# Optimization experiments

Measured on AMD Instinct MI355X. Metric: run time of the kernel, lower is better.

Reference implementation:

```python
import jax, jax.numpy as jnp
import numpy as np

B, T, C, H = 4, 2048, 768, 12
D = C // H

def setup_inputs() -> dict:
    key = jax.random.key(0)
    ks = jax.random.split(key, 8)
    s = 1.0 / np.sqrt(C)
    return {
        "x":  jax.random.normal(ks[0], (B, T, C), dtype=jnp.float32),
        "Wq": jax.random.normal(ks[1], (C, C), dtype=jnp.float32) * s,
        "bq": jax.random.normal(ks[2], (C,), dtype=jnp.float32) * 0.02,
        "Wk": jax.random.normal(ks[3], (C, C), dtype=jnp.float32) * s,
        "bk": jax.random.normal(ks[4], (C,), dtype=jnp.float32) * 0.02,
        "Wv": jax.random.normal(ks[5], (C, C), dtype=jnp.float32) * s,
        "bv": jax.random.normal(ks[6], (C,), dtype=jnp.float32) * 0.02,
        "Wp": jax.random.normal(ks[7], (C, C), dtype=jnp.float32) * s,
    }

def reference(x, Wq, bq, Wk, bk, Wv, bv, Wp):
    # Linear projections (torch Linear: y = x @ W.T + b)
    q = x @ Wq.T + bq
    k = x @ Wk.T + bk
    v = x @ Wv.T + bv
    # [B,T,C] -> [B,H,T,D]
    q = q.reshape(B, T, H, D).transpose(0, 2, 1, 3)
    k = k.reshape(B, T, H, D).transpose(0, 2, 1, 3)
    v = v.reshape(B, T, H, D).transpose(0, 2, 1, 3)
    scale = 1.0 / np.sqrt(D).astype(np.float32)
    scores = jnp.einsum('bhqd,bhkd->bhqk', q, k) * scale  # [B,H,T,T]
    attn = jax.nn.softmax(scores, axis=-1)  # no mask in original module
    out = jnp.einsum('bhqk,bhkd->bhqd', attn, v)
    out = out.transpose(0, 2, 1, 3).reshape(B, T, C)
    return out @ Wp.T  # proj has bias=False
```

## Files before the change

kernel.cpp:

```cpp
#include <hip/hip_runtime.h>
#include <hip/hip_bf16.h>
#include <cmath>

constexpr int B  = 4;
constexpr int T  = 2048;
constexpr int C  = 768;
constexpr int H  = 12;
constexpr int Dh = 64;
constexpr int M  = B * T;
constexpr int NQKV = 3 * C;
constexpr int WS2  = C * C;

typedef short bf16x8 __attribute__((ext_vector_type(8)));
typedef short bf16x4 __attribute__((ext_vector_type(4)));
typedef float f32x4  __attribute__((ext_vector_type(4)));
typedef float f32x16 __attribute__((ext_vector_type(16)));

constexpr float SOFT_SCALE = 0.18033688011112042f;

__device__ inline short f2bf(float f) {
    unsigned u = __float_as_uint(f);
    u += 0x7fffu + ((u >> 16) & 1u);
    return (short)(u >> 16);
}

__device__ inline unsigned pk_bf16(float a, float b) {
    __hip_bfloat162 h = __float22bfloat162_rn(float2{a, b});
    return *(unsigned*)&h;
}

__device__ inline bf16x8 mk8(unsigned a, unsigned b, unsigned c, unsigned d) {
    union { unsigned u[4]; bf16x8 v; } x;
    x.u[0] = a; x.u[1] = b; x.u[2] = c; x.u[3] = d;
    return x.v;
}

typedef const __attribute__((address_space(1))) unsigned GU;
typedef __attribute__((address_space(3))) unsigned LU;
__device__ inline void async_copy16(const void* g, void* l) {
    __builtin_amdgcn_global_load_lds((GU*)g, (LU*)l, 16, 0, 0);
}

constexpr size_t XE = (size_t)M * C;
constexpr size_t CV_TOTAL = XE + 4 * (size_t)WS2;

__global__ __launch_bounds__(256)
void convert_all(const float* __restrict__ x,  const float* __restrict__ Wq,
                 const float* __restrict__ Wk, const float* __restrict__ Wv,
                 const float* __restrict__ Wp,
                 short* __restrict__ xb, short* __restrict__ Wqkv,
                 short* __restrict__ Wpb) {
    size_t i = ((size_t)blockIdx.x * 256 + threadIdx.x) * 4;
    const float* src; short* dst; size_t off;
    if (i < XE)                        { src = x;  dst = xb;            off = i; }
    else if (i < XE + WS2)             { src = Wq; dst = Wqkv;          off = i - XE; }
    else if (i < XE + 2 * (size_t)WS2) { src = Wk; dst = Wqkv + WS2;    off = i - XE - WS2; }
    else if (i < XE + 3 * (size_t)WS2) { src = Wv; dst = Wqkv + 2 * WS2; off = i - XE - 2 * (size_t)WS2; }
    else                               { src = Wp; dst = Wpb;           off = i - XE - 3 * (size_t)WS2; }
    float4 v = *(const float4*)(src + off);
    bf16x4 o; o[0] = f2bf(v.x); o[1] = f2bf(v.y); o[2] = f2bf(v.z); o[3] = f2bf(v.w);
    *(bf16x4*)(dst + off) = o;
}

constexpr int BM = 128;
constexpr int MTILES = M / BM;

template<int BN_, int WMW, int WNW, int OUT_BF16, int QSCALE>
__global__ __launch_bounds__(256)
void gemm_bt(const short* __restrict__ A, const short* __restrict__ W,
             const float* __restrict__ bias0, const float* __restrict__ bias1,
             const float* __restrict__ bias2,
             void* __restrict__ Yv, int Ndim, int Kdim) {
    constexpr int MT  = BM / WMW / 16;
    constexpr int NT  = BN_ / WNW / 16;
    constexpr int NCH = (BM + BN_) / 16;

    __shared__ short As[2][BM * 32];
    __shared__ short Bs[2][BN_ * 32];

    const int tid  = threadIdx.x;
    const int wave = tid >> 6;
    const int lane = tid & 63;
    const int li   = lane & 15;
    const int quad = lane >> 4;
    const int wm   = wave % WMW;
    const int wn   = wave / WMW;

    const int ntiles = Ndim / BN_;
    const int bid  = blockIdx.x;
    const int xcd  = bid & 7;
    const int idx  = bid >> 3;
    const int mloc = idx / ntiles;
    const int ntt  = idx % ntiles;
    const int m0   = (xcd * (MTILES / 8) + mloc) * BM;
    const int n0   = ntt * BN_;

    f32x4 acc[MT][NT];
    #pragma unroll
    for (int i = 0; i < MT; ++i)
        #pragma unroll
        for (int j = 0; j < NT; ++j)
            acc[i][j] = (f32x4){0.f, 0.f, 0.f, 0.f};

    const int lrow = lane >> 2;
    const int lkof = (lane & 3) * 8;

    for (int k0 = 0; k0 < Kdim; k0 += 64) {
        __syncthreads();
        #pragma unroll
        for (int h = 0; h < 2; ++h)
            #pragma unroll
            for (int ii = 0; ii < NCH / 4; ++ii) {
                int c = ii * 4 + wave;
                if (c < BM / 16)
                    async_copy16(A + (size_t)(m0 + c * 16 + lrow) * Kdim
                                   + k0 + h * 32 + lkof,
                                 &As[h][c * 512]);
                else
                    async_copy16(W + (size_t)(n0 + (c - BM / 16) * 16 + lrow) * Kdim
                                   + k0 + h * 32 + lkof,
                                 &Bs[h][(c - BM / 16) * 512]);
            }
        __syncthreads();

        #pragma unroll
        for (int h = 0; h < 2; ++h) {
            bf16x8 af[MT], bfr[NT];
            #pragma unroll
            for (int t = 0; t < MT; ++t)
                af[t] = *(const bf16x8*)&As[h][(wm * MT * 16 + t * 16 + li) * 32 + quad * 8];
            #pragma unroll
            for (int t = 0; t < NT; ++t)
                bfr[t] = *(const bf16x8*)&Bs[h][(wn * NT * 16 + t * 16 + li) * 32 + quad * 8];
            #pragma unroll
            for (int i = 0; i < MT; ++i)
                #pragma unroll
                for (int j = 0; j < NT; ++j)
                    acc[i][j] = __builtin_amdgcn_mfma_f32_16x16x32_bf16(
                        af[i], bfr[j], acc[i][j], 0, 0, 0);
        }
    }

    float bb[NT];
    #pragma unroll
    for (int nt = 0; nt < NT; ++nt) bb[nt] = 0.f;
    if (bias0) {
        int s = n0 / C;
        const float* bp = (s == 0) ? bias0 : ((s == 1) ? bias1 : bias2);
        int nb = n0 % C;
        #pragma unroll
        for (int nt = 0; nt < NT; ++nt)
            bb[nt] = bp[nb + wn * NT * 16 + nt * 16 + li];
    }

    #pragma unroll
    for (int mt = 0; mt < MT; ++mt)
        #pragma unroll
        for (int nt = 0; nt < NT; ++nt)
            #pragma unroll
            for (int r = 0; r < 4; ++r) {
                int row = m0 + wm * MT * 16 + mt * 16 + quad * 4 + r;
                int col = n0 + wn * NT * 16 + nt * 16 + li;
                float v = acc[mt][nt][r] + bb[nt];
                if constexpr (QSCALE) {
                    if (n0 < C) v *= SOFT_SCALE;
                }
                if constexpr (OUT_BF16)
                    ((short*)Yv)[(size_t)row * Ndim + col] = f2bf(v);
                else
                    ((float*)Yv)[(size_t)row * Ndim + col] = v;
            }
}

constexpr int QT   = 128;
constexpr int KTT  = 64;
constexpr int LSTR = 72;
constexpr int QS   = NQKV;

__global__ __launch_bounds__(256, 3)
void attn_fwd(const short* __restrict__ QKV, short* __restrict__ O) {
    __shared__ short Ks0[KTT * LSTR];
    __shared__ short Ks1[KTT * LSTR];
    __shared__ short Vt0[Dh * LSTR];
    __shared__ short Vt1[Dh * LSTR];

    const int tid  = threadIdx.x;
    const int wave = tid >> 6;
    const int lane = tid & 63;
    const int r31  = lane & 31;
    const int hi   = lane >> 5;

    const int bid   = blockIdx.x;
    const int xcd   = bid & 7;
    const int idx   = bid >> 3;
    const int gloc  = idx >> 4;
    const int qt    = idx & 15;
    const int group = xcd * 6 + gloc;
    const int b     = group / H;
    const int h     = group % H;
    const int qw    = qt * QT + wave * 32;

    const short* Qg = QKV + (size_t)(b * T) * QS + h * Dh;
    const short* Kg = QKV + (size_t)(b * T) * QS + C + h * Dh;
    const short* Vg = QKV + (size_t)(b * T) * QS + 2 * C + h * Dh;

    bf16x8 qf[4];
    #pragma unroll
    for (int f = 0; f < 4; ++f)
        qf[f] = *(const bf16x8*)(Qg + (size_t)(qw + r31) * QS + f * 16 + hi * 8);

    bf16x8 ones;
    #pragma unroll
    for (int i = 0; i < 8; ++i) ones[i] = (short)0x3F80;

    f32x16 oacc0 = (f32x16)(0.f);
    f32x16 oacc1 = (f32x16)(0.f);
    f32x16 lacc  = (f32x16)(0.f);

    const int ktok = tid >> 3;
    const int kch  = tid & 7;
    const int vd2  = (tid & 31) * 2;
    const int vg   = tid >> 5;

    int4 kpre[2];
    unsigned vpre[8];

    auto load_regs = [&](int kt0) {
        kpre[0] = *(const int4*)(Kg + (size_t)(kt0 + ktok)      * QS + kch * 8);
        kpre[1] = *(const int4*)(Kg + (size_t)(kt0 + ktok + 32) * QS + kch * 8);
        #pragma unroll
        for (int t2 = 0; t2 < 8; ++t2)
            vpre[t2] = *(const unsigned*)(Vg + (size_t)(kt0 + vg * 8 + t2) * QS + vd2);
    };
    auto write_tile = [&](short (&KsT)[KTT * LSTR], short (&VtT)[Dh * LSTR]) {
        *(int4*)&KsT[ktok * LSTR + kch * 8]        = kpre[0];
        *(int4*)&KsT[(ktok + 32) * LSTR + kch * 8] = kpre[1];
        unsigned lo[4], hh[4];
        #pragma unroll
        for (int j = 0; j < 4; ++j) {
            lo[j] = __builtin_amdgcn_perm(vpre[2 * j + 1], vpre[2 * j], 0x05040100u);
            hh[j] = __builtin_amdgcn_perm(vpre[2 * j + 1], vpre[2 * j], 0x07060302u);
        }
        *(int4*)&VtT[vd2 * LSTR + vg * 8]       = make_int4(lo[0], lo[1], lo[2], lo[3]);
        *(int4*)&VtT[(vd2 + 1) * LSTR + vg * 8] = make_int4(hh[0], hh[1], hh[2], hh[3]);
    };

    auto half_iter = [&](const short (&KsT)[KTT * LSTR], const short (&VtT)[Dh * LSTR],
                         short (&KsN)[KTT * LSTR], short (&VtN)[Dh * LSTR],
                         bool do_stage, int next_load) {
        __syncthreads();

        f32x16 st0 = (f32x16)(0.f);
        f32x16 st1 = (f32x16)(0.f);
        __builtin_amdgcn_s_setprio(1);
        #pragma unroll
        for (int f = 0; f < 4; ++f) {
            bf16x8 k0 = *(const bf16x8*)&KsT[(r31)      * LSTR + f * 16 + hi * 8];
            bf16x8 k1 = *(const bf16x8*)&KsT[(32 + r31) * LSTR + f * 16 + hi * 8];
            st0 = __builtin_amdgcn_mfma_f32_32x32x16_bf16(k0, qf[f], st0, 0, 0, 0);
            st1 = __builtin_amdgcn_mfma_f32_32x32x16_bf16(k1, qf[f], st1, 0, 0, 0);
        }
        __builtin_amdgcn_s_setprio(0);

        if (do_stage)       write_tile(KsN, VtN);
        if (next_load >= 0) load_regs(next_load);

        #pragma unroll
        for (int kb = 0; kb < 2; ++kb) {
            f32x16 s = kb ? st1 : st0;
            unsigned d[8];
            #pragma unroll
            for (int j = 0; j < 8; ++j) {
                float pa = __builtin_amdgcn_exp2f(s[2 * j]);
                float pb = __builtin_amdgcn_exp2f(s[2 * j + 1]);
                d[j] = pk_bf16(pa, pb);
            }
            auto s02 = __builtin_amdgcn_permlane32_swap(d[0], d[2], false, false);
            auto s13 = __builtin_amdgcn_permlane32_swap(d[1], d[3], false, false);
            auto s46 = __builtin_amdgcn_permlane32_swap(d[4], d[6], false, false);
            auto s57 = __builtin_amdgcn_permlane32_swap(d[5], d[7], false, false);
            bf16x8 pf0 = mk8(s02[0], s13[0], s02[1], s13[1]);
            bf16x8 pf1 = mk8(s46[0], s57[0], s46[1], s57[1]);

            __builtin_amdgcn_s_setprio(1);
            lacc = __builtin_amdgcn_mfma_f32_32x32x16_bf16(pf0, ones, lacc, 0, 0, 0);
            lacc = __builtin_amdgcn_mfma_f32_32x32x16_bf16(pf1, ones, lacc, 0, 0, 0);

            bf16x8 v00 = *(const bf16x8*)&VtT[(r31)      * LSTR + kb * 32 + hi * 8];
            bf16x8 v01 = *(const bf16x8*)&VtT[(r31)      * LSTR + kb * 32 + 16 + hi * 8];
            bf16x8 v10 = *(const bf16x8*)&VtT[(32 + r31) * LSTR + kb * 32 + hi * 8];
            bf16x8 v11 = *(const bf16x8*)&VtT[(32 + r31) * LSTR + kb * 32 + 16 + hi * 8];
            oacc0 = __builtin_amdgcn_mfma_f32_32x32x16_bf16(pf0, v00, oacc0, 0, 0, 0);
            oacc0 = __builtin_amdgcn_mfma_f32_32x32x16_bf16(pf1, v01, oacc0, 0, 0, 0);
            oacc1 = __builtin_amdgcn_mfma_f32_32x32x16_bf16(pf0, v10, oacc1, 0, 0, 0);
            oacc1 = __builtin_amdgcn_mfma_f32_32x32x16_bf16(pf1, v11, oacc1, 0, 0, 0);
            __builtin_amdgcn_s_setprio(0);
        }
    };

    load_regs(0);
    write_tile(Ks0, Vt0);
    load_regs(KTT);

    for (int kt = 0; kt < T; kt += 2 * KTT) {
        half_iter(Ks0, Vt0, Ks1, Vt1, true,
                  (kt + 2 * KTT < T) ? kt + 2 * KTT : -1);
        half_iter(Ks1, Vt1, Ks0, Vt0, kt + 2 * KTT < T,
                  (kt + 3 * KTT < T) ? kt + 3 * KTT : -1);
    }

    #pragma unroll
    for (int r = 0; r < 16; ++r) {
        float inv = 1.0f / lacc[r];
        int row = (r & 3) + 8 * (r >> 2) + 4 * hi;
        short* op = O + (size_t)(b * T + qw + row) * C + h * Dh + r31;
        op[0]  = f2bf(oacc0[r] * inv);
        op[32] = f2bf(oacc1[r] * inv);
    }
}

extern "C" void kernel_launch(void* const* d_in, const int* in_sizes, int n_in,
                              void* d_out, int out_size, void* d_ws, size_t ws_size,
                              hipStream_t stream) {
    (void)in_sizes; (void)n_in; (void)out_size; (void)ws_size;

    const float* x  = (const float*)d_in[0];
    const float* Wq = (const float*)d_in[1];
    const float* bq = (const float*)d_in[2];
    const float* Wk = (const float*)d_in[3];
    const float* bk = (const float*)d_in[4];
    const float* Wv = (const float*)d_in[5];
    const float* bv = (const float*)d_in[6];
    const float* Wp = (const float*)d_in[7];
    float* out = (float*)d_out;

    short* xb    = (short*)d_ws;
    short* Wqkv  = xb + (size_t)M * C;
    short* Wpb   = Wqkv + 3 * (size_t)WS2;
    short* QKVb  = Wpb + (size_t)WS2;
    short* AOb   = QKVb + (size_t)M * NQKV;

    convert_all<<<dim3(CV_TOTAL / 1024), 256, 0, stream>>>(
        x, Wq, Wk, Wv, Wp, xb, Wqkv, Wpb);

    gemm_bt<128, 2, 2, 1, 1><<<dim3(MTILES * (NQKV / 128)), 256, 0, stream>>>(
        xb, Wqkv, bq, bk, bv, QKVb, NQKV, C);

    attn_fwd<<<dim3((T / QT) * H * B), 256, 0, stream>>>(QKVb, AOb);

    gemm_bt<64, 4, 1, 0, 0><<<dim3(MTILES * (C / 64)), 256, 0, stream>>>(
        AOb, Wpb, nullptr, nullptr, nullptr, out, C, C);
}
```

Before: 232.3 us.

## Add 256x256-tile QKV GEMM kernel with 512 threads and XCD-aware block mapping

Replaces the generic 128-tile QKV projection GEMM with a dedicated kernel that uses 256x256 output tiles, 8 waves, double-buffered async LDS staging over 64-wide K chunks, and a block-to-tile mapping that groups M-rows per XCD. Larger tiles raise arithmetic intensity and cut redundant global loads of A and W, and the XCD grouping aims to improve L2 locality. The trade-offs are heavy LDS use (128 KB per block) and high register pressure from 32 accumulators per wave, which limit occupancy, plus only 288 blocks to spread across the CUs.

```diff
diff --git a/kernel.cpp b/kernel.cpp
--- a/kernel.cpp
+++ b/kernel.cpp
@@ -172,6 +172,110 @@
             }
 }
 
+__global__ __launch_bounds__(512, 2)
+void gemm_qkv256(const short* __restrict__ A, const short* __restrict__ W,
+                 const float* __restrict__ bias0, const float* __restrict__ bias1,
+                 const float* __restrict__ bias2,
+                 short* __restrict__ Y) {
+    constexpr int Kdim = C;
+    constexpr int Ndim = NQKV;
+    constexpr int MT = 8, NT = 4;
+
+    __shared__ short As0[2][256 * 32];
+    __shared__ short As1[2][256 * 32];
+    __shared__ short Bs0[2][256 * 32];
+    __shared__ short Bs1[2][256 * 32];
+
+    const int tid  = threadIdx.x;
+    const int wave = tid >> 6;
+    const int lane = tid & 63;
+    const int li   = lane & 15;
+    const int quad = lane >> 4;
+    const int wm   = wave >> 2;
+    const int wn   = wave & 3;
+
+    const int bid  = blockIdx.x;
+    const int xcd  = bid & 7;
+    const int idx  = bid >> 3;
+    const int m0   = (xcd * 4 + idx / 9) * 256;
+    const int n0   = (idx % 9) * 256;
+
+    f32x4 acc[MT][NT];
+    #pragma unroll
+    for (int i = 0; i < MT; ++i)
+        #pragma unroll
+        for (int j = 0; j < NT; ++j)
+            acc[i][j] = (f32x4){0.f, 0.f, 0.f, 0.f};
+
+    const int grow = tid >> 2;
+    const int gcol = (tid & 3) * 8;
+    auto stage = [&](short (&Ad)[2][256 * 32], short (&Bd)[2][256 * 32], int k0) {
+        #pragma unroll
+        for (int h = 0; h < 2; ++h)
+            #pragma unroll
+            for (int r = 0; r < 2; ++r) {
+                async_copy16(A + (size_t)(m0 + r * 128 + grow) * Kdim
+                               + k0 + h * 32 + gcol,
+                             &Ad[h][(r * 128 + wave * 16) * 32]);
+                async_copy16(W + (size_t)(n0 + r * 128 + grow) * Kdim
+                               + k0 + h * 32 + gcol,
+                             &Bd[h][(r * 128 + wave * 16) * 32]);
+            }
+    };
+
+    auto compute = [&](const short (&Ad)[2][256 * 32],
+                       const short (&Bd)[2][256 * 32]) {
+        #pragma unroll
+        for (int h = 0; h < 2; ++h) {
+            bf16x8 af[MT], bfr[NT];
+            #pragma unroll
+            for (int t = 0; t < MT; ++t)
+                af[t] = *(const bf16x8*)&Ad[h][(wm * 128 + t * 16 + li) * 32 + quad * 8];
+            #pragma unroll
+            for (int t = 0; t < NT; ++t)
+                bfr[t] = *(const bf16x8*)&Bd[h][(wn * 64 + t * 16 + li) * 32 + quad * 8];
+            #pragma unroll
+            for (int i = 0; i < MT; ++i)
+                #pragma unroll
+                for (int j = 0; j < NT; ++j)
+                    acc[i][j] = __builtin_amdgcn_mfma_f32_16x16x32_bf16(
+                        af[i], bfr[j], acc[i][j], 0, 0, 0);
+        }
+    };
+
+    stage(As0, Bs0, 0);
+    for (int i = 0; i < 6; ++i) {
+        const int k0 = i * 128;
+        __syncthreads();
+        stage(As1, Bs1, k0 + 64);
+        compute(As0, Bs0);
+        __syncthreads();
+        if (i < 5) stage(As0, Bs0, k0 + 128);
+        compute(As1, Bs1);
+    }
+
+    const int s  = n0 / C;
+    const float* bp = (s == 0) ? bias0 : ((s == 1) ? bias1 : bias2);
+    const int nb = n0 % C;
+    float bb[NT];
+    #pragma unroll
+    for (int nt = 0; nt < NT; ++nt)
+        bb[nt] = bp[nb + wn * 64 + nt * 16 + li];
+
+    #pragma unroll
+    for (int mt = 0; mt < MT; ++mt)
+        #pragma unroll
+        for (int nt = 0; nt < NT; ++nt)
+            #pragma unroll
+            for (int r = 0; r < 4; ++r) {
+                int row = m0 + wm * 128 + mt * 16 + quad * 4 + r;
+                int col = n0 + wn * 64 + nt * 16 + li;
+                float v = acc[mt][nt][r] + bb[nt];
+                if (n0 < C) v *= SOFT_SCALE;
+                Y[(size_t)row * Ndim + col] = f2bf(v);
+            }
+}
+
 constexpr int QT   = 128;
 constexpr int KTT  = 64;
 constexpr int LSTR = 72;
@@ -343,8 +447,8 @@
     convert_all<<<dim3(CV_TOTAL / 1024), 256, 0, stream>>>(
         x, Wq, Wk, Wv, Wp, xb, Wqkv, Wpb);
 
-    gemm_bt<128, 2, 2, 1, 1><<<dim3(MTILES * (NQKV / 128)), 256, 0, stream>>>(
-        xb, Wqkv, bq, bk, bv, QKVb, NQKV, C);
+    gemm_qkv256<<<dim3(288), 512, 0, stream>>>(
+        xb, Wqkv, bq, bk, bv, QKVb);
 
     attn_fwd<<<dim3((T / QT) * H * B), 256, 0, stream>>>(QKVb, AOb);
 
```

After: 240.8 us. 1.04x slower.

## Give each attention wave two 32-row query groups, halving block size

Applied to the files above, without the earlier changes.

The attention kernel now runs 2 waves per block instead of 4, and each wave handles 64 query rows as two 32-row groups. Each K and V fragment read from LDS is reused across both groups, which cuts LDS reads per unit of MFMA work. The K/V staging loads per thread double to keep the same 64-token tile. The cost is higher register pressure, since accumulators and Q fragments double, and fewer waves per block to hide latency.

```diff
diff --git a/kernel.cpp b/kernel.cpp
--- a/kernel.cpp
+++ b/kernel.cpp
@@ -177,7 +177,7 @@
 constexpr int LSTR = 72;
 constexpr int QS   = NQKV;
 
-__global__ __launch_bounds__(256, 3)
+__global__ __launch_bounds__(128, 2)
 void attn_fwd(const short* __restrict__ QKV, short* __restrict__ O) {
     __shared__ short Ks0[KTT * LSTR];
     __shared__ short Ks1[KTT * LSTR];
@@ -198,51 +198,62 @@
     const int group = xcd * 6 + gloc;
     const int b     = group / H;
     const int h     = group % H;
-    const int qw    = qt * QT + wave * 32;
+    const int qw    = qt * QT + wave * 64;
 
     const short* Qg = QKV + (size_t)(b * T) * QS + h * Dh;
     const short* Kg = QKV + (size_t)(b * T) * QS + C + h * Dh;
     const short* Vg = QKV + (size_t)(b * T) * QS + 2 * C + h * Dh;
 
-    bf16x8 qf[4];
-    #pragma unroll
-    for (int f = 0; f < 4; ++f)
-        qf[f] = *(const bf16x8*)(Qg + (size_t)(qw + r31) * QS + f * 16 + hi * 8);
+    bf16x8 qf[2][4];
+    #pragma unroll
+    for (int qg = 0; qg < 2; ++qg)
+        #pragma unroll
+        for (int f = 0; f < 4; ++f)
+            qf[qg][f] = *(const bf16x8*)(Qg + (size_t)(qw + qg * 32 + r31) * QS
+                                            + f * 16 + hi * 8);
 
     bf16x8 ones;
     #pragma unroll
     for (int i = 0; i < 8; ++i) ones[i] = (short)0x3F80;
 
-    f32x16 oacc0 = (f32x16)(0.f);
-    f32x16 oacc1 = (f32x16)(0.f);
-    f32x16 lacc  = (f32x16)(0.f);
+    f32x16 oacc0[2], oacc1[2], lacc[2];
+    #pragma unroll
+    for (int qg = 0; qg < 2; ++qg) {
+        oacc0[qg] = (f32x16)(0.f);
+        oacc1[qg] = (f32x16)(0.f);
+        lacc[qg]  = (f32x16)(0.f);
+    }
 
     const int ktok = tid >> 3;
     const int kch  = tid & 7;
     const int vd2  = (tid & 31) * 2;
     const int vg   = tid >> 5;
 
-    int4 kpre[2];
-    unsigned vpre[8];
+    int4 kpre[4];
+    unsigned vpre[16];
 
     auto load_regs = [&](int kt0) {
-        kpre[0] = *(const int4*)(Kg + (size_t)(kt0 + ktok)      * QS + kch * 8);
-        kpre[1] = *(const int4*)(Kg + (size_t)(kt0 + ktok + 32) * QS + kch * 8);
-        #pragma unroll
-        for (int t2 = 0; t2 < 8; ++t2)
-            vpre[t2] = *(const unsigned*)(Vg + (size_t)(kt0 + vg * 8 + t2) * QS + vd2);
+        #pragma unroll
+        for (int r = 0; r < 4; ++r)
+            kpre[r] = *(const int4*)(Kg + (size_t)(kt0 + ktok + r * 16) * QS + kch * 8);
+        #pragma unroll
+        for (int t2 = 0; t2 < 16; ++t2)
+            vpre[t2] = *(const unsigned*)(Vg + (size_t)(kt0 + vg * 16 + t2) * QS + vd2);
     };
     auto write_tile = [&](short (&KsT)[KTT * LSTR], short (&VtT)[Dh * LSTR]) {
-        *(int4*)&KsT[ktok * LSTR + kch * 8]        = kpre[0];
-        *(int4*)&KsT[(ktok + 32) * LSTR + kch * 8] = kpre[1];
-        unsigned lo[4], hh[4];
-        #pragma unroll
-        for (int j = 0; j < 4; ++j) {
+        #pragma unroll
+        for (int r = 0; r < 4; ++r)
+            *(int4*)&KsT[(ktok + r * 16) * LSTR + kch * 8] = kpre[r];
+        unsigned lo[8], hh[8];
+        #pragma unroll
+        for (int j = 0; j < 8; ++j) {
             lo[j] = __builtin_amdgcn_perm(vpre[2 * j + 1], vpre[2 * j], 0x05040100u);
             hh[j] = __builtin_amdgcn_perm(vpre[2 * j + 1], vpre[2 * j], 0x07060302u);
         }
-        *(int4*)&VtT[vd2 * LSTR + vg * 8]       = make_int4(lo[0], lo[1], lo[2], lo[3]);
-        *(int4*)&VtT[(vd2 + 1) * LSTR + vg * 8] = make_int4(hh[0], hh[1], hh[2], hh[3]);
+        *(int4*)&VtT[vd2 * LSTR + vg * 16]           = make_int4(lo[0], lo[1], lo[2], lo[3]);
+        *(int4*)&VtT[vd2 * LSTR + vg * 16 + 8]       = make_int4(lo[4], lo[5], lo[6], lo[7]);
+        *(int4*)&VtT[(vd2 + 1) * LSTR + vg * 16]     = make_int4(hh[0], hh[1], hh[2], hh[3]);
+        *(int4*)&VtT[(vd2 + 1) * LSTR + vg * 16 + 8] = make_int4(hh[4], hh[5], hh[6], hh[7]);
     };
 
     auto half_iter = [&](const short (&KsT)[KTT * LSTR], const short (&VtT)[Dh * LSTR],
@@ -250,51 +261,56 @@
                          bool do_stage, int next_load) {
         __syncthreads();
 
-        f32x16 st0 = (f32x16)(0.f);
-        f32x16 st1 = (f32x16)(0.f);
-        __builtin_amdgcn_s_setprio(1);
-        #pragma unroll
-        for (int f = 0; f < 4; ++f) {
-            bf16x8 k0 = *(const bf16x8*)&KsT[(r31)      * LSTR + f * 16 + hi * 8];
-            bf16x8 k1 = *(const bf16x8*)&KsT[(32 + r31) * LSTR + f * 16 + hi * 8];
-            st0 = __builtin_amdgcn_mfma_f32_32x32x16_bf16(k0, qf[f], st0, 0, 0, 0);
-            st1 = __builtin_amdgcn_mfma_f32_32x32x16_bf16(k1, qf[f], st1, 0, 0, 0);
-        }
-        __builtin_amdgcn_s_setprio(0);
-
-        if (do_stage)       write_tile(KsN, VtN);
-        if (next_load >= 0) load_regs(next_load);
-
-        #pragma unroll
-        for (int kb = 0; kb < 2; ++kb) {
-            f32x16 s = kb ? st1 : st0;
-            unsigned d[8];
-            #pragma unroll
-            for (int j = 0; j < 8; ++j) {
-                float pa = __builtin_amdgcn_exp2f(s[2 * j]);
-                float pb = __builtin_amdgcn_exp2f(s[2 * j + 1]);
-                d[j] = pk_bf16(pa, pb);
-            }
-            auto s02 = __builtin_amdgcn_permlane32_swap(d[0], d[2], false, false);
-            auto s13 = __builtin_amdgcn_permlane32_swap(d[1], d[3], false, false);
-            auto s46 = __builtin_amdgcn_permlane32_swap(d[4], d[6], false, false);
-            auto s57 = __builtin_amdgcn_permlane32_swap(d[5], d[7], false, false);
-            bf16x8 pf0 = mk8(s02[0], s13[0], s02[1], s13[1]);
-            bf16x8 pf1 = mk8(s46[0], s57[0], s46[1], s57[1]);
-
+        #pragma unroll
+        for (int qg = 0; qg < 2; ++qg) {
+            f32x16 st0 = (f32x16)(0.f);
+            f32x16 st1 = (f32x16)(0.f);
             __builtin_amdgcn_s_setprio(1);
-            lacc = __builtin_amdgcn_mfma_f32_32x32x16_bf16(pf0, ones, lacc, 0, 0, 0);
-            lacc = __builtin_amdgcn_mfma_f32_32x32x16_bf16(pf1, ones, lacc, 0, 0, 0);
-
-            bf16x8 v00 = *(const bf16x8*)&VtT[(r31)      * LSTR + kb * 32 + hi * 8];
-            bf16x8 v01 = *(const bf16x8*)&VtT[(r31)      * LSTR + kb * 32 + 16 + hi * 8];
-            bf16x8 v10 = *(const bf16x8*)&VtT[(32 + r31) * LSTR + kb * 32 + hi * 8];
-            bf16x8 v11 = *(const bf16x8*)&VtT[(32 + r31) * LSTR + kb * 32 + 16 + hi * 8];
-            oacc0 = __builtin_amdgcn_mfma_f32_32x32x16_bf16(pf0, v00, oacc0, 0, 0, 0);
-            oacc0 = __builtin_amdgcn_mfma_f32_32x32x16_bf16(pf1, v01, oacc0, 0, 0, 0);
-            oacc1 = __builtin_amdgcn_mfma_f32_32x32x16_bf16(pf0, v10, oacc1, 0, 0, 0);
-            oacc1 = __builtin_amdgcn_mfma_f32_32x32x16_bf16(pf1, v11, oacc1, 0, 0, 0);
+            #pragma unroll
+            for (int f = 0; f < 4; ++f) {
+                bf16x8 k0 = *(const bf16x8*)&KsT[(r31)      * LSTR + f * 16 + hi * 8];
+                bf16x8 k1 = *(const bf16x8*)&KsT[(32 + r31) * LSTR + f * 16 + hi * 8];
+                st0 = __builtin_amdgcn_mfma_f32_32x32x16_bf16(k0, qf[qg][f], st0, 0, 0, 0);
+                st1 = __builtin_amdgcn_mfma_f32_32x32x16_bf16(k1, qf[qg][f], st1, 0, 0, 0);
+            }
             __builtin_amdgcn_s_setprio(0);
+
+            if (qg == 0) {
+                if (do_stage)       write_tile(KsN, VtN);
+                if (next_load >= 0) load_regs(next_load);
+            }
+
+            #pragma unroll
+            for (int kb = 0; kb < 2; ++kb) {
+                f32x16 s = kb ? st1 : st0;
+                unsigned d[8];
+                #pragma unroll
+                for (int j = 0; j < 8; ++j) {
+                    float pa = __builtin_amdgcn_exp2f(s[2 * j]);
+                    float pb = __builtin_amdgcn_exp2f(s[2 * j + 1]);
+                    d[j] = pk_bf16(pa, pb);
+                }
+                auto s02 = __builtin_amdgcn_permlane32_swap(d[0], d[2], false, false);
+                auto s13 = __builtin_amdgcn_permlane32_swap(d[1], d[3], false, false);
+                auto s46 = __builtin_amdgcn_permlane32_swap(d[4], d[6], false, false);
+                auto s57 = __builtin_amdgcn_permlane32_swap(d[5], d[7], false, false);
+                bf16x8 pf0 = mk8(s02[0], s13[0], s02[1], s13[1]);
+                bf16x8 pf1 = mk8(s46[0], s57[0], s46[1], s57[1]);
+
+                __builtin_amdgcn_s_setprio(1);
+                lacc[qg] = __builtin_amdgcn_mfma_f32_32x32x16_bf16(pf0, ones, lacc[qg], 0, 0, 0);
+                lacc[qg] = __builtin_amdgcn_mfma_f32_32x32x16_bf16(pf1, ones, lacc[qg], 0, 0, 0);
+
+                bf16x8 v00 = *(const bf16x8*)&VtT[(r31)      * LSTR + kb * 32 + hi * 8];
+                bf16x8 v01 = *(const bf16x8*)&VtT[(r31)      * LSTR + kb * 32 + 16 + hi * 8];
+                bf16x8 v10 = *(const bf16x8*)&VtT[(32 + r31) * LSTR + kb * 32 + hi * 8];
+                bf16x8 v11 = *(const bf16x8*)&VtT[(32 + r31) * LSTR + kb * 32 + 16 + hi * 8];
+                oacc0[qg] = __builtin_amdgcn_mfma_f32_32x32x16_bf16(pf0, v00, oacc0[qg], 0, 0, 0);
+                oacc0[qg] = __builtin_amdgcn_mfma_f32_32x32x16_bf16(pf1, v01, oacc0[qg], 0, 0, 0);
+                oacc1[qg] = __builtin_amdgcn_mfma_f32_32x32x16_bf16(pf0, v10, oacc1[qg], 0, 0, 0);
+                oacc1[qg] = __builtin_amdgcn_mfma_f32_32x32x16_bf16(pf1, v11, oacc1[qg], 0, 0, 0);
+                __builtin_amdgcn_s_setprio(0);
+            }
         }
     };
 
@@ -310,13 +326,15 @@
     }
 
     #pragma unroll
-    for (int r = 0; r < 16; ++r) {
-        float inv = 1.0f / lacc[r];
-        int row = (r & 3) + 8 * (r >> 2) + 4 * hi;
-        short* op = O + (size_t)(b * T + qw + row) * C + h * Dh + r31;
-        op[0]  = f2bf(oacc0[r] * inv);
-        op[32] = f2bf(oacc1[r] * inv);
-    }
+    for (int qg = 0; qg < 2; ++qg)
+        #pragma unroll
+        for (int r = 0; r < 16; ++r) {
+            float inv = 1.0f / lacc[qg][r];
+            int row = (r & 3) + 8 * (r >> 2) + 4 * hi;
+            short* op = O + (size_t)(b * T + qw + qg * 32 + row) * C + h * Dh + r31;
+            op[0]  = f2bf(oacc0[qg][r] * inv);
+            op[32] = f2bf(oacc1[qg][r] * inv);
+        }
 }
 
 extern "C" void kernel_launch(void* const* d_in, const int* in_sizes, int n_in,
@@ -346,7 +364,7 @@
     gemm_bt<128, 2, 2, 1, 1><<<dim3(MTILES * (NQKV / 128)), 256, 0, stream>>>(
         xb, Wqkv, bq, bk, bv, QKVb, NQKV, C);
 
-    attn_fwd<<<dim3((T / QT) * H * B), 256, 0, stream>>>(QKVb, AOb);
+    attn_fwd<<<dim3((T / QT) * H * B), 128, 0, stream>>>(QKVb, AOb);
 
     gemm_bt<64, 4, 1, 0, 0><<<dim3(MTILES * (C / 64)), 256, 0, stream>>>(
         AOb, Wpb, nullptr, nullptr, nullptr, out, C, C);
```

New measurement: 254.8 us. 9.7% more time.
